# Kernel optimization log

Measured on AMD Instinct MI355X. Metric: run time of the kernel, lower is better.

Reference implementation:

```python
import jax, jax.numpy as jnp
import numpy as np

THRESH = 0.01


def _grid_adj(H, W):
    """4-neighbor grid adjacency with self loops, (N,N) float32."""
    N = H * W
    A = np.eye(N, dtype=np.float32)
    idx = np.arange(N).reshape(H, W)
    A[idx[1:, :].ravel(), idx[:-1, :].ravel()] = 1.0   # up neighbor
    A[idx[:-1, :].ravel(), idx[1:, :].ravel()] = 1.0   # down neighbor
    A[idx[:, 1:].ravel(), idx[:, :-1].ravel()] = 1.0   # left neighbor
    A[idx[:, :-1].ravel(), idx[:, 1:].ravel()] = 1.0   # right neighbor
    return jnp.asarray(A)


def setup_inputs() -> dict:
    key = jax.random.key(0)
    kx, k1, k2, k3, k4 = jax.random.split(key, 5)
    B, C, H, W = 8, 256, 48, 48
    scale = 1.0 / np.sqrt(C)  # keep QK^T logits in a sane range
    return {
        "x": jax.random.normal(kx, (B, C, H, W), dtype=jnp.float32),
        "phi_w": jax.random.normal(k1, (C, C), dtype=jnp.float32) * scale,
        "psi_w": jax.random.normal(k2, (C, C), dtype=jnp.float32) * scale,
        "w0_w": jax.random.normal(k3, (C, C), dtype=jnp.float32) * scale,
        "w1_w": jax.random.normal(k4, (C, C), dtype=jnp.float32) * scale,
    }


def reference(x, phi_w, psi_w, w0_w, w1_w):
    B, C, H, W = x.shape
    N = H * W
    A_base = _grid_adj(H, W)                      # (N, N), static
    X = jnp.transpose(x, (0, 2, 3, 1)).reshape(B, N, C)  # (B, N, C)
    Q = jnp.einsum('bnc,dc->bnd', X, phi_w)       # Linear(no bias): X @ W^T
    K = jnp.einsum('bnc,dc->bnd', X, psi_w)
    S = jax.nn.softmax(jnp.einsum('bnd,bmd->bnm', Q, K), axis=2)  # (B,N,N)
    S = jnp.where(S < THRESH, 0.0, S)
    A = A_base[None, :, :] + S                    # (B, N, N)
    diagA = jnp.diagonal(A, axis1=1, axis2=2)     # (B, N)
    m0 = jnp.einsum('bnc,dc->bnd', X * diagA[..., None], w0_w)
    eye = jnp.eye(N, dtype=x.dtype)
    A_off = A * (1.0 - eye)[None, :, :]
    nbr_msg = jnp.einsum('bnm,bmc->bnc', A_off, X)
    m1 = jnp.einsum('bnc,dc->bnd', nbr_msg, w1_w)
    Y = jax.nn.relu(m0 + m1)                      # (B, N, C_out)
    return jnp.transpose(Y.reshape(B, H, W, -1), (0, 3, 1, 2))
```

## Files before the change

### kernel.cpp

```cpp
#include <hip/hip_runtime.h>

#define HWDIM 48
#define NPIX 2304
#define CDIM 256
#define BATCH 8
#define THRESH 0.01f
#define SHIFT 90.0f

typedef _Float16 f16;
typedef _Float16 f16x8 __attribute__((ext_vector_type(8)));
typedef float f32x4 __attribute__((ext_vector_type(4)));

#define MFMA16(a, b, c) __builtin_amdgcn_mfma_f32_16x16x32_f16(a, b, c, 0, 0, 0)

__global__ __launch_bounds__(256) void prep_kernel(const float* __restrict__ x,
                                                   const float* __restrict__ phi,
                                                   const float* __restrict__ psi,
                                                   const float* __restrict__ w0,
                                                   const float* __restrict__ w1,
                                                   f16* __restrict__ Xh,
                                                   f16* __restrict__ Xc,
                                                   f16* __restrict__ wH) {
    if (blockIdx.z == BATCH) {
        int bid = blockIdx.y * gridDim.x + blockIdx.x;
        int t = bid * 256 + threadIdx.x;
        for (int i = t; i < 4 * CDIM * CDIM; i += 576 * 256) {
            const float* src = (i < 65536) ? phi : (i < 131072) ? psi
                               : (i < 196608) ? w0 : w1;
            wH[i] = (f16)src[i & 65535];
        }
        return;
    }
    __shared__ float tile[32][33];
    int b = blockIdx.z;
    int n0 = blockIdx.x * 32, c0 = blockIdx.y * 32;
    int tx = threadIdx.x & 31, ty = threadIdx.x >> 5;
    const float* xb = x + (size_t)b * CDIM * NPIX;
    f16* XcB = Xc + (size_t)b * CDIM * NPIX;
    f16* XhB = Xh + (size_t)b * NPIX * CDIM;
#pragma unroll
    for (int j = 0; j < 4; ++j) {
        int c = c0 + ty + 8 * j;
        float v = xb[(size_t)c * NPIX + n0 + tx];
        tile[ty + 8 * j][tx] = v;
        XcB[(size_t)c * NPIX + n0 + tx] = (f16)v;
    }
    __syncthreads();
#pragma unroll
    for (int j = 0; j < 4; ++j) {
        int n = n0 + ty + 8 * j;
        XhB[(size_t)n * CDIM + c0 + tx] = (f16)tile[tx][ty + 8 * j];
    }
}

__global__ __launch_bounds__(256) void proj_kernel(const f16* __restrict__ Xh,
                                                   const f16* __restrict__ wH,
                                                   f16* __restrict__ Qh,
                                                   f16* __restrict__ Kh) {
    __shared__ f16 ot[64 * 264];
    int b = blockIdx.y;
    int n0 = blockIdx.x * 64;
    const f16* Wp = wH + (size_t)blockIdx.z * CDIM * CDIM;
    f16* dst = blockIdx.z ? Kh : Qh;
    int tid = threadIdx.x;
    int l = tid & 63, w = tid >> 6;
    int wr = w >> 1, dw = w & 1;
    int lr = l & 15, lg = l >> 4;
    const f16* Xb = Xh + (size_t)b * NPIX * CDIM;

    f32x4 acc[2][8];
#pragma unroll
    for (int rs = 0; rs < 2; ++rs)
#pragma unroll
        for (int dt = 0; dt < 8; ++dt) acc[rs][dt] = {0.f, 0.f, 0.f, 0.f};

#pragma unroll
    for (int ks = 0; ks < 8; ++ks) {
        f16x8 a0 = *(const f16x8*)(Xb + (size_t)(n0 + wr * 32 + lr) * CDIM + ks * 32 + lg * 8);
        f16x8 a1 = *(const f16x8*)(Xb + (size_t)(n0 + wr * 32 + 16 + lr) * CDIM + ks * 32 + lg * 8);
#pragma unroll
        for (int dt = 0; dt < 8; ++dt) {
            f16x8 bf = *(const f16x8*)(Wp + (size_t)(dw * 128 + dt * 16 + lr) * CDIM + ks * 32 + lg * 8);
            acc[0][dt] = MFMA16(a0, bf, acc[0][dt]);
            acc[1][dt] = MFMA16(a1, bf, acc[1][dt]);
        }
    }
#pragma unroll
    for (int rs = 0; rs < 2; ++rs)
#pragma unroll
        for (int dt = 0; dt < 8; ++dt)
#pragma unroll
            for (int reg = 0; reg < 4; ++reg)
                ot[(wr * 32 + rs * 16 + lg * 4 + reg) * 264 + dw * 128 + dt * 16 + lr] =
                    (f16)acc[rs][dt][reg];
    __syncthreads();
#pragma unroll
    for (int rep = 0; rep < 8; ++rep) {
        int flat = rep * 256 + tid;
        int r = flat >> 5, seg = flat & 31;
        *(f16x8*)(dst + (size_t)(b * NPIX + n0 + r) * CDIM + seg * 8) =
            *(const f16x8*)(ot + r * 264 + seg * 8);
    }
}

__global__ __launch_bounds__(256) void statsA_kernel(const f16* __restrict__ Qh,
                                                     const f16* __restrict__ Kh,
                                                     f16* __restrict__ Lh,
                                                     float* __restrict__ invZ,
                                                     float* __restrict__ diagT) {
    __shared__ f16 Lds[32][72];
    __shared__ float zpart[4][32];
    __shared__ float diagbuf[32];
    int b = blockIdx.y;
    int n0 = blockIdx.x * 32;
    int tid = threadIdx.x;
    int l = tid & 63, cw = tid >> 6;
    int lr = l & 15, lg = l >> 4;
    const f16* Qb = Qh + (size_t)b * NPIX * CDIM;
    const f16* Kb = Kh + (size_t)b * NPIX * CDIM;
    f16* Lb = Lh + (size_t)b * NPIX * NPIX;
    int strow = tid >> 3, stseg = tid & 7;

    f16x8 qa[2][8];
#pragma unroll
    for (int rs = 0; rs < 2; ++rs)
#pragma unroll
        for (int ks = 0; ks < 8; ++ks)
            qa[rs][ks] = *(const f16x8*)(Qb + (size_t)(n0 + rs * 16 + lr) * CDIM + ks * 32 + lg * 8);

    float zs[2][4] = {{0.f, 0.f, 0.f, 0.f}, {0.f, 0.f, 0.f, 0.f}};
#pragma unroll 1
    for (int mt = 0; mt < 36; ++mt) {
        int m0 = mt * 64;
        f32x4 acc[2] = {{0.f, 0.f, 0.f, 0.f}, {0.f, 0.f, 0.f, 0.f}};
#pragma unroll
        for (int ks = 0; ks < 8; ++ks) {
            f16x8 bf = *(const f16x8*)(Kb + (size_t)(m0 + cw * 16 + lr) * CDIM + ks * 32 + lg * 8);
            acc[0] = MFMA16(qa[0][ks], bf, acc[0]);
            acc[1] = MFMA16(qa[1][ks], bf, acc[1]);
        }
#pragma unroll
        for (int rs = 0; rs < 2; ++rs)
#pragma unroll
            for (int reg = 0; reg < 4; ++reg) {
                int row32 = rs * 16 + lg * 4 + reg;
                f16 lh = (f16)acc[rs][reg];
                Lds[row32][cw * 16 + lr] = lh;
                float e = __expf((float)lh - SHIFT);
                zs[rs][reg] += e;
                if (m0 + cw * 16 + lr == n0 + row32) diagbuf[row32] = e;
            }
        __syncthreads();
        *(f16x8*)(Lb + (size_t)(n0 + strow) * NPIX + m0 + stseg * 8) =
            *(const f16x8*)(&Lds[strow][stseg * 8]);
        __syncthreads();
    }
#pragma unroll
    for (int rs = 0; rs < 2; ++rs)
#pragma unroll
        for (int reg = 0; reg < 4; ++reg) {
            float v = zs[rs][reg];
            v += __shfl_xor(v, 1);
            v += __shfl_xor(v, 2);
            v += __shfl_xor(v, 4);
            v += __shfl_xor(v, 8);
            zs[rs][reg] = v;
        }
    if (lr == 0)
#pragma unroll
        for (int rs = 0; rs < 2; ++rs)
#pragma unroll
            for (int reg = 0; reg < 4; ++reg)
                zpart[cw][rs * 16 + lg * 4 + reg] = zs[rs][reg];
    __syncthreads();
    if (tid < 32) {
        float Z = zpart[0][tid] + zpart[1][tid] + zpart[2][tid] + zpart[3][tid];
        float iz = 1.0f / Z;
        int n = b * NPIX + n0 + tid;
        invZ[n] = iz;
        float d = diagbuf[tid] * iz;
        diagT[n] = (d < THRESH) ? 0.0f : d;
    }
}

__global__ __launch_bounds__(256) void g_kernel(const float* __restrict__ x,
                                                const float* __restrict__ diagT,
                                                f16* __restrict__ Gh) {
    __shared__ float tile[32][33];
    int b = blockIdx.z;
    int n0 = blockIdx.x * 32, c0 = blockIdx.y * 32;
    int tx = threadIdx.x & 31, ty = threadIdx.x >> 5;
    const float* xb = x + (size_t)b * CDIM * NPIX;
#pragma unroll
    for (int j = 0; j < 4; ++j) {
        int c = c0 + ty + 8 * j;
        int n = n0 + tx;
        int hh = n / HWDIM, ww = n % HWDIM;
        const float* row = xb + (size_t)c * NPIX;
        float v = -diagT[b * NPIX + n] * row[n];
        if (hh > 0)         v += row[n - HWDIM];
        if (hh < HWDIM - 1) v += row[n + HWDIM];
        if (ww > 0)         v += row[n - 1];
        if (ww < HWDIM - 1) v += row[n + 1];
        tile[ty + 8 * j][tx] = v;
    }
    __syncthreads();
#pragma unroll
    for (int j = 0; j < 4; ++j) {
        int n = n0 + ty + 8 * j;
        Gh[((size_t)b * NPIX + n) * CDIM + c0 + tx] = (f16)tile[tx][ty + 8 * j];
    }
}

__global__ __launch_bounds__(256) void nbrB_kernel(const f16* __restrict__ Lh,
                                                   const f16* __restrict__ Xc,
                                                   const float* __restrict__ invZ,
                                                   const f16* __restrict__ Gh,
                                                   f16* __restrict__ nbrH) {
    __shared__ f16 Tls[32][72];
    __shared__ f16 ot[32][264];
    int b = blockIdx.y;
    int n0 = blockIdx.x * 32;
    int tid = threadIdx.x;
    int l = tid & 63, cwq = tid >> 6;
    int lr = l & 15, lg = l >> 4;
    const f16* Lb = Lh + (size_t)b * NPIX * NPIX;
    const f16* Xb = Xc + (size_t)b * CDIM * NPIX;
    int ldrow = tid >> 3, ldseg = tid & 7;
    float iz = invZ[b * NPIX + n0 + ldrow];

    f32x4 acc[2][4];
#pragma unroll
    for (int rs = 0; rs < 2; ++rs)
#pragma unroll
        for (int ct = 0; ct < 4; ++ct) acc[rs][ct] = {0.f, 0.f, 0.f, 0.f};

    f16x8 lv = *(const f16x8*)(Lb + (size_t)(n0 + ldrow) * NPIX + ldseg * 8);
#pragma unroll 1
    for (int mt = 0; mt < 36; ++mt) {
        int m0 = mt * 64;
        f16x8 tv;
#pragma unroll
        for (int j = 0; j < 8; ++j) {
            float s = __expf((float)lv[j] - SHIFT) * iz;
            tv[j] = (f16)((s < THRESH) ? 0.0f : s);
        }
        __syncthreads();
        *(f16x8*)(&Tls[ldrow][ldseg * 8]) = tv;
        if (mt < 35)
            lv = *(const f16x8*)(Lb + (size_t)(n0 + ldrow) * NPIX + (m0 + 64) + ldseg * 8);
        __syncthreads();
#pragma unroll
        for (int kk = 0; kk < 2; ++kk) {
            f16x8 af0 = *(const f16x8*)(&Tls[lr][kk * 32 + lg * 8]);
            f16x8 af1 = *(const f16x8*)(&Tls[16 + lr][kk * 32 + lg * 8]);
#pragma unroll
            for (int ct = 0; ct < 4; ++ct) {
                f16x8 bf = *(const f16x8*)(Xb + (size_t)(cwq * 64 + ct * 16 + lr) * NPIX + m0 + kk * 32 + lg * 8);
                acc[0][ct] = MFMA16(af0, bf, acc[0][ct]);
                acc[1][ct] = MFMA16(af1, bf, acc[1][ct]);
            }
        }
    }
#pragma unroll
    for (int rs = 0; rs < 2; ++rs)
#pragma unroll
        for (int ct = 0; ct < 4; ++ct)
#pragma unroll
            for (int reg = 0; reg < 4; ++reg) {
                int row32 = rs * 16 + lg * 4 + reg;
                int c = cwq * 64 + ct * 16 + lr;
                float v = acc[rs][ct][reg] +
                          (float)Gh[((size_t)b * NPIX + n0 + row32) * CDIM + c];
                ot[row32][c] = (f16)v;
            }
    __syncthreads();
#pragma unroll
    for (int rep = 0; rep < 4; ++rep) {
        int id = rep * 256 + tid;
        int r = id >> 5, seg = id & 31;
        *(f16x8*)(nbrH + (size_t)(b * NPIX + n0 + r) * CDIM + seg * 8) =
            *(const f16x8*)(&ot[r][seg * 8]);
    }
}

__global__ __launch_bounds__(256) void final_kernel(const f16* __restrict__ Xh,
                                                    const f16* __restrict__ nbrH,
                                                    const f16* __restrict__ wH,
                                                    const float* __restrict__ diagT,
                                                    float* __restrict__ out) {
    int b = blockIdx.y;
    int n0 = blockIdx.x * 64;
    int tid = threadIdx.x;
    int l = tid & 63, w = tid >> 6;
    int wr = w >> 1, dw = w & 1;
    int lr = l & 15, lg = l >> 4;
    const f16* Xb = Xh + (size_t)b * NPIX * CDIM;
    const f16* Nb = nbrH + (size_t)b * NPIX * CDIM;
    const f16* w0H = wH + 2 * CDIM * CDIM;
    const f16* w1H = wH + 3 * CDIM * CDIM;

    f32x4 acc[2][8];
#pragma unroll
    for (int rs = 0; rs < 2; ++rs)
#pragma unroll
        for (int dt = 0; dt < 8; ++dt) acc[rs][dt] = {0.f, 0.f, 0.f, 0.f};

#pragma unroll
    for (int ks = 0; ks < 8; ++ks) {
        f16x8 a0 = *(const f16x8*)(Xb + (size_t)(n0 + wr * 32 + lr) * CDIM + ks * 32 + lg * 8);
        f16x8 a1 = *(const f16x8*)(Xb + (size_t)(n0 + wr * 32 + 16 + lr) * CDIM + ks * 32 + lg * 8);
#pragma unroll
        for (int dt = 0; dt < 8; ++dt) {
            f16x8 bf = *(const f16x8*)(w0H + (size_t)(dw * 128 + dt * 16 + lr) * CDIM + ks * 32 + lg * 8);
            acc[0][dt] = MFMA16(a0, bf, acc[0][dt]);
            acc[1][dt] = MFMA16(a1, bf, acc[1][dt]);
        }
    }
#pragma unroll
    for (int rs = 0; rs < 2; ++rs)
#pragma unroll
        for (int reg = 0; reg < 4; ++reg) {
            int n = n0 + wr * 32 + rs * 16 + lg * 4 + reg;
            float s = 1.0f + diagT[b * NPIX + n];
#pragma unroll
            for (int dt = 0; dt < 8; ++dt) acc[rs][dt][reg] *= s;
        }
#pragma unroll
    for (int ks = 0; ks < 8; ++ks) {
        f16x8 a0 = *(const f16x8*)(Nb + (size_t)(n0 + wr * 32 + lr) * CDIM + ks * 32 + lg * 8);
        f16x8 a1 = *(const f16x8*)(Nb + (size_t)(n0 + wr * 32 + 16 + lr) * CDIM + ks * 32 + lg * 8);
#pragma unroll
        for (int dt = 0; dt < 8; ++dt) {
            f16x8 bf = *(const f16x8*)(w1H + (size_t)(dw * 128 + dt * 16 + lr) * CDIM + ks * 32 + lg * 8);
            acc[0][dt] = MFMA16(a0, bf, acc[0][dt]);
            acc[1][dt] = MFMA16(a1, bf, acc[1][dt]);
        }
    }
#pragma unroll
    for (int rs = 0; rs < 2; ++rs)
#pragma unroll
        for (int dt = 0; dt < 8; ++dt) {
            int d = dw * 128 + dt * 16 + lr;
            int nb_ = n0 + wr * 32 + rs * 16 + lg * 4;
            f32x4 v = acc[rs][dt];
#pragma unroll
            for (int reg = 0; reg < 4; ++reg) v[reg] = fmaxf(v[reg], 0.0f);
            *(f32x4*)(out + ((size_t)b * CDIM + d) * NPIX + nb_) = v;
        }
}

extern "C" void kernel_launch(void* const* d_in, const int* in_sizes, int n_in,
                              void* d_out, int out_size, void* d_ws, size_t ws_size,
                              hipStream_t stream) {
    const float* x   = (const float*)d_in[0];
    const float* phi = (const float*)d_in[1];
    const float* psi = (const float*)d_in[2];
    const float* w0  = (const float*)d_in[3];
    const float* w1  = (const float*)d_in[4];
    float* out = (float*)d_out;

    const size_t BNC = (size_t)BATCH * NPIX * CDIM;
    char* p = (char*)d_ws;
    auto alloc = [&](size_t bytes) { char* r = p; p += (bytes + 255) & ~(size_t)255; return r; };
    f16*   Xh    = (f16*)alloc(BNC * 2);
    f16*   Xc    = (f16*)alloc(BNC * 2);
    f16*   Qh    = (f16*)alloc(BNC * 2);
    f16*   Kh    = (f16*)alloc(BNC * 2);
    f16*   nbrH  = (f16*)alloc(BNC * 2);
    f16*   Gh    = (f16*)alloc(BNC * 2);
    f16*   wH    = (f16*)alloc((size_t)4 * CDIM * CDIM * 2);
    float* invZ  = (float*)alloc((size_t)BATCH * NPIX * 4);
    float* diagT = (float*)alloc((size_t)BATCH * NPIX * 4);
    f16*   Lh    = (f16*)alloc((size_t)BATCH * NPIX * NPIX * 2);

    prep_kernel<<<dim3(72, 8, 9), 256, 0, stream>>>(x, phi, psi, w0, w1, Xh, Xc, wH);
    proj_kernel<<<dim3(36, 8, 2), 256, 0, stream>>>(Xh, wH, Qh, Kh);
    statsA_kernel<<<dim3(72, 8), 256, 0, stream>>>(Qh, Kh, Lh, invZ, diagT);
    g_kernel<<<dim3(72, 8, 8), 256, 0, stream>>>(x, diagT, Gh);
    nbrB_kernel<<<dim3(72, 8), 256, 0, stream>>>(Lh, Xc, invZ, Gh, nbrH);
    final_kernel<<<dim3(36, 8), 256, 0, stream>>>(Xh, nbrH, wH, diagT, out);
}
```

Measured before the change: 391.2 us.

## Replace dense thresholded attention matrix with per-row sparse lists from recomputed logits

The stats kernel no longer writes the full fp16 logit matrix. It runs a second QK^T pass once the softmax normaliser is known and records only entries with probability at least the threshold into per-row lists. The cap of 104 per row is safe because at most 100 softmax values can reach 0.01. A new sparse kernel gathers those neighbour rows of X and accumulates them, replacing the dense MFMA aggregation and the separate channel-major copy of X. This removes a large intermediate round trip and the dense N×N product. The cost is doing QK^T twice, plus shared-memory atomics and scalar gather loads.

```diff
diff --git a/kernel.cpp b/kernel.cpp
--- a/kernel.cpp
+++ b/kernel.cpp
@@ -6,12 +6,20 @@
 #define BATCH 8
 #define THRESH 0.01f
 #define SHIFT 90.0f
+#define LISTCAP 104
 
 typedef _Float16 f16;
 typedef _Float16 f16x8 __attribute__((ext_vector_type(8)));
 typedef float f32x4 __attribute__((ext_vector_type(4)));
 
 #define MFMA16(a, b, c) __builtin_amdgcn_mfma_f32_16x16x32_f16(a, b, c, 0, 0, 0)
+
+static __device__ __forceinline__ unsigned short f16bits(f16 v) {
+    return __builtin_bit_cast(unsigned short, v);
+}
+static __device__ __forceinline__ f16 bits2f16(unsigned short u) {
+    return __builtin_bit_cast(f16, u);
+}
 
 __global__ __launch_bounds__(256) void prep_kernel(const float* __restrict__ x,
                                                    const float* __restrict__ phi,
@@ -19,7 +27,6 @@
                                                    const float* __restrict__ w0,
                                                    const float* __restrict__ w1,
                                                    f16* __restrict__ Xh,
-                                                   f16* __restrict__ Xc,
                                                    f16* __restrict__ wH) {
     if (blockIdx.z == BATCH) {
         int bid = blockIdx.y * gridDim.x + blockIdx.x;
@@ -36,14 +43,11 @@
     int n0 = blockIdx.x * 32, c0 = blockIdx.y * 32;
     int tx = threadIdx.x & 31, ty = threadIdx.x >> 5;
     const float* xb = x + (size_t)b * CDIM * NPIX;
-    f16* XcB = Xc + (size_t)b * CDIM * NPIX;
     f16* XhB = Xh + (size_t)b * NPIX * CDIM;
 #pragma unroll
     for (int j = 0; j < 4; ++j) {
         int c = c0 + ty + 8 * j;
-        float v = xb[(size_t)c * NPIX + n0 + tx];
-        tile[ty + 8 * j][tx] = v;
-        XcB[(size_t)c * NPIX + n0 + tx] = (f16)v;
+        tile[ty + 8 * j][tx] = xb[(size_t)c * NPIX + n0 + tx];
     }
     __syncthreads();
 #pragma unroll
@@ -103,14 +107,18 @@
     }
 }
 
-__global__ __launch_bounds__(256) void statsA_kernel(const f16* __restrict__ Qh,
-                                                     const f16* __restrict__ Kh,
-                                                     f16* __restrict__ Lh,
-                                                     float* __restrict__ invZ,
-                                                     float* __restrict__ diagT) {
-    __shared__ f16 Lds[32][72];
+__global__ __launch_bounds__(256) void statsAB_kernel(const f16* __restrict__ Qh,
+                                                      const f16* __restrict__ Kh,
+                                                      float* __restrict__ invZ,
+                                                      float* __restrict__ diagT,
+                                                      unsigned* __restrict__ lists,
+                                                      int* __restrict__ cnts) {
     __shared__ float zpart[4][32];
     __shared__ float diagbuf[32];
+    __shared__ float invZ_s[32];
+    __shared__ float thr_s[32];
+    __shared__ int cnt_s[32];
+    __shared__ unsigned list_s[32][LISTCAP];
     int b = blockIdx.y;
     int n0 = blockIdx.x * 32;
     int tid = threadIdx.x;
@@ -118,8 +126,8 @@
     int lr = l & 15, lg = l >> 4;
     const f16* Qb = Qh + (size_t)b * NPIX * CDIM;
     const f16* Kb = Kh + (size_t)b * NPIX * CDIM;
-    f16* Lb = Lh + (size_t)b * NPIX * NPIX;
-    int strow = tid >> 3, stseg = tid & 7;
+
+    if (tid < 32) cnt_s[tid] = 0;
 
     f16x8 qa[2][8];
 #pragma unroll
@@ -144,16 +152,10 @@
 #pragma unroll
             for (int reg = 0; reg < 4; ++reg) {
                 int row32 = rs * 16 + lg * 4 + reg;
-                f16 lh = (f16)acc[rs][reg];
-                Lds[row32][cw * 16 + lr] = lh;
-                float e = __expf((float)lh - SHIFT);
+                float e = __expf(acc[rs][reg] - SHIFT);
                 zs[rs][reg] += e;
                 if (m0 + cw * 16 + lr == n0 + row32) diagbuf[row32] = e;
             }
-        __syncthreads();
-        *(f16x8*)(Lb + (size_t)(n0 + strow) * NPIX + m0 + stseg * 8) =
-            *(const f16x8*)(&Lds[strow][stseg * 8]);
-        __syncthreads();
     }
 #pragma unroll
     for (int rs = 0; rs < 2; ++rs)
@@ -176,11 +178,60 @@
     if (tid < 32) {
         float Z = zpart[0][tid] + zpart[1][tid] + zpart[2][tid] + zpart[3][tid];
         float iz = 1.0f / Z;
+        invZ_s[tid] = iz;
+        thr_s[tid] = logf(THRESH) - logf(iz) - 1e-3f;
         int n = b * NPIX + n0 + tid;
         invZ[n] = iz;
         float d = diagbuf[tid] * iz;
         diagT[n] = (d < THRESH) ? 0.0f : d;
     }
+    __syncthreads();
+
+    float thrv[2][4], izv[2][4];
+#pragma unroll
+    for (int rs = 0; rs < 2; ++rs)
+#pragma unroll
+        for (int reg = 0; reg < 4; ++reg) {
+            int row32 = rs * 16 + lg * 4 + reg;
+            thrv[rs][reg] = thr_s[row32];
+            izv[rs][reg] = invZ_s[row32];
+        }
+
+#pragma unroll 1
+    for (int mt = 0; mt < 36; ++mt) {
+        int m0 = mt * 64;
+        f32x4 acc[2] = {{0.f, 0.f, 0.f, 0.f}, {0.f, 0.f, 0.f, 0.f}};
+#pragma unroll
+        for (int ks = 0; ks < 8; ++ks) {
+            f16x8 bf = *(const f16x8*)(Kb + (size_t)(m0 + cw * 16 + lr) * CDIM + ks * 32 + lg * 8);
+            acc[0] = MFMA16(qa[0][ks], bf, acc[0]);
+            acc[1] = MFMA16(qa[1][ks], bf, acc[1]);
+        }
+#pragma unroll
+        for (int rs = 0; rs < 2; ++rs)
+#pragma unroll
+            for (int reg = 0; reg < 4; ++reg) {
+                float lm = acc[rs][reg] - SHIFT;
+                if (lm >= thrv[rs][reg]) {
+                    float s = __expf(lm) * izv[rs][reg];
+                    if (s >= THRESH) {
+                        int row32 = rs * 16 + lg * 4 + reg;
+                        int idx = atomicAdd(&cnt_s[row32], 1);
+                        if (idx < LISTCAP)
+                            list_s[row32][idx] =
+                                ((unsigned)(m0 + cw * 16 + lr) << 16) | f16bits((f16)s);
+                    }
+                }
+            }
+    }
+    __syncthreads();
+    if (tid < 32) {
+        int c = cnt_s[tid];
+        cnts[b * NPIX + n0 + tid] = (c > LISTCAP) ? LISTCAP : c;
+    }
+    unsigned* lblk = lists + (size_t)(b * NPIX + n0) * LISTCAP;
+    const unsigned* lsrc = &list_s[0][0];
+    for (int i = tid; i < 32 * LISTCAP; i += 256) lblk[i] = lsrc[i];
 }
 
 __global__ __launch_bounds__(256) void g_kernel(const float* __restrict__ x,
@@ -212,76 +263,36 @@
     }
 }
 
-__global__ __launch_bounds__(256) void nbrB_kernel(const f16* __restrict__ Lh,
-                                                   const f16* __restrict__ Xc,
-                                                   const float* __restrict__ invZ,
-                                                   const f16* __restrict__ Gh,
-                                                   f16* __restrict__ nbrH) {
-    __shared__ f16 Tls[32][72];
-    __shared__ f16 ot[32][264];
+__global__ __launch_bounds__(256) void sparse_kernel(const unsigned* __restrict__ lists,
+                                                     const int* __restrict__ cnts,
+                                                     const f16* __restrict__ Xh,
+                                                     const f16* __restrict__ Gh,
+                                                     f16* __restrict__ nbrH) {
     int b = blockIdx.y;
     int n0 = blockIdx.x * 32;
     int tid = threadIdx.x;
-    int l = tid & 63, cwq = tid >> 6;
-    int lr = l & 15, lg = l >> 4;
-    const f16* Lb = Lh + (size_t)b * NPIX * NPIX;
-    const f16* Xb = Xc + (size_t)b * CDIM * NPIX;
-    int ldrow = tid >> 3, ldseg = tid & 7;
-    float iz = invZ[b * NPIX + n0 + ldrow];
-
-    f32x4 acc[2][4];
-#pragma unroll
-    for (int rs = 0; rs < 2; ++rs)
-#pragma unroll
-        for (int ct = 0; ct < 4; ++ct) acc[rs][ct] = {0.f, 0.f, 0.f, 0.f};
-
-    f16x8 lv = *(const f16x8*)(Lb + (size_t)(n0 + ldrow) * NPIX + ldseg * 8);
-#pragma unroll 1
-    for (int mt = 0; mt < 36; ++mt) {
-        int m0 = mt * 64;
-        f16x8 tv;
-#pragma unroll
-        for (int j = 0; j < 8; ++j) {
-            float s = __expf((float)lv[j] - SHIFT) * iz;
-            tv[j] = (f16)((s < THRESH) ? 0.0f : s);
-        }
-        __syncthreads();
-        *(f16x8*)(&Tls[ldrow][ldseg * 8]) = tv;
-        if (mt < 35)
-            lv = *(const f16x8*)(Lb + (size_t)(n0 + ldrow) * NPIX + (m0 + 64) + ldseg * 8);
-        __syncthreads();
-#pragma unroll
-        for (int kk = 0; kk < 2; ++kk) {
-            f16x8 af0 = *(const f16x8*)(&Tls[lr][kk * 32 + lg * 8]);
-            f16x8 af1 = *(const f16x8*)(&Tls[16 + lr][kk * 32 + lg * 8]);
-#pragma unroll
-            for (int ct = 0; ct < 4; ++ct) {
-                f16x8 bf = *(const f16x8*)(Xb + (size_t)(cwq * 64 + ct * 16 + lr) * NPIX + m0 + kk * 32 + lg * 8);
-                acc[0][ct] = MFMA16(af0, bf, acc[0][ct]);
-                acc[1][ct] = MFMA16(af1, bf, acc[1][ct]);
-            }
-        }
-    }
-#pragma unroll
-    for (int rs = 0; rs < 2; ++rs)
-#pragma unroll
-        for (int ct = 0; ct < 4; ++ct)
-#pragma unroll
-            for (int reg = 0; reg < 4; ++reg) {
-                int row32 = rs * 16 + lg * 4 + reg;
-                int c = cwq * 64 + ct * 16 + lr;
-                float v = acc[rs][ct][reg] +
-                          (float)Gh[((size_t)b * NPIX + n0 + row32) * CDIM + c];
-                ot[row32][c] = (f16)v;
-            }
-    __syncthreads();
-#pragma unroll
-    for (int rep = 0; rep < 4; ++rep) {
-        int id = rep * 256 + tid;
-        int r = id >> 5, seg = id & 31;
-        *(f16x8*)(nbrH + (size_t)(b * NPIX + n0 + r) * CDIM + seg * 8) =
-            *(const f16x8*)(&ot[r][seg * 8]);
-    }
+    int r = tid >> 3, t8 = tid & 7;
+    int n = n0 + r;
+    const f16* Xb = Xh + (size_t)b * NPIX * CDIM;
+    int k = cnts[b * NPIX + n];
+    const unsigned* lrow = lists + (size_t)(b * NPIX + n) * LISTCAP;
+
+    float accv[32];
+#pragma unroll
+    for (int j = 0; j < 32; ++j) accv[j] = 0.f;
+
+    for (int i = 0; i < k; ++i) {
+        unsigned pk = lrow[i];
+        int m = pk >> 16;
+        float s = (float)bits2f16((unsigned short)(pk & 0xffffu));
+        const f16* xr = Xb + (size_t)m * CDIM + t8 * 32;
+#pragma unroll
+        for (int j = 0; j < 32; ++j) accv[j] += s * (float)xr[j];
+    }
+    const f16* gr = Gh + ((size_t)b * NPIX + n) * CDIM + t8 * 32;
+    f16* orow = nbrH + ((size_t)b * NPIX + n) * CDIM + t8 * 32;
+#pragma unroll
+    for (int j = 0; j < 32; ++j) orow[j] = (f16)(accv[j] + (float)gr[j]);
 }
 
 __global__ __launch_bounds__(256) void final_kernel(const f16* __restrict__ Xh,
@@ -361,23 +372,24 @@
     float* out = (float*)d_out;
 
     const size_t BNC = (size_t)BATCH * NPIX * CDIM;
+    const size_t BN  = (size_t)BATCH * NPIX;
     char* p = (char*)d_ws;
     auto alloc = [&](size_t bytes) { char* r = p; p += (bytes + 255) & ~(size_t)255; return r; };
-    f16*   Xh    = (f16*)alloc(BNC * 2);
-    f16*   Xc    = (f16*)alloc(BNC * 2);
-    f16*   Qh    = (f16*)alloc(BNC * 2);
-    f16*   Kh    = (f16*)alloc(BNC * 2);
-    f16*   nbrH  = (f16*)alloc(BNC * 2);
-    f16*   Gh    = (f16*)alloc(BNC * 2);
-    f16*   wH    = (f16*)alloc((size_t)4 * CDIM * CDIM * 2);
-    float* invZ  = (float*)alloc((size_t)BATCH * NPIX * 4);
-    float* diagT = (float*)alloc((size_t)BATCH * NPIX * 4);
-    f16*   Lh    = (f16*)alloc((size_t)BATCH * NPIX * NPIX * 2);
-
-    prep_kernel<<<dim3(72, 8, 9), 256, 0, stream>>>(x, phi, psi, w0, w1, Xh, Xc, wH);
+    f16*      Xh    = (f16*)alloc(BNC * 2);
+    f16*      Qh    = (f16*)alloc(BNC * 2);
+    f16*      Kh    = (f16*)alloc(BNC * 2);
+    f16*      nbrH  = (f16*)alloc(BNC * 2);
+    f16*      Gh    = (f16*)alloc(BNC * 2);
+    f16*      wH    = (f16*)alloc((size_t)4 * CDIM * CDIM * 2);
+    float*    invZ  = (float*)alloc(BN * 4);
+    float*    diagT = (float*)alloc(BN * 4);
+    unsigned* lists = (unsigned*)alloc(BN * LISTCAP * 4);
+    int*      cnts  = (int*)alloc(BN * 4);
+
+    prep_kernel<<<dim3(72, 8, 9), 256, 0, stream>>>(x, phi, psi, w0, w1, Xh, wH);
     proj_kernel<<<dim3(36, 8, 2), 256, 0, stream>>>(Xh, wH, Qh, Kh);
-    statsA_kernel<<<dim3(72, 8), 256, 0, stream>>>(Qh, Kh, Lh, invZ, diagT);
+    statsAB_kernel<<<dim3(72, 8), 256, 0, stream>>>(Qh, Kh, invZ, diagT, lists, cnts);
     g_kernel<<<dim3(72, 8, 8), 256, 0, stream>>>(x, diagT, Gh);
-    nbrB_kernel<<<dim3(72, 8), 256, 0, stream>>>(Lh, Xc, invZ, Gh, nbrH);
+    sparse_kernel<<<dim3(72, 8), 256, 0, stream>>>(lists, cnts, Xh, Gh, nbrH);
     final_kernel<<<dim3(36, 8), 256, 0, stream>>>(Xh, nbrH, wH, diagT, out);
 }
```

Result: faster. 380.6 us (-2.7%).
